# Kernel optimization log

Measured on AMD Instinct MI355X. Metric: run time of the kernel, lower is better.

Reference implementation:

```python
import jax, jax.numpy as jnp
import numpy as np

D = 128          # node_embed_size
N_NODES = 100000
E = 600000       # edges per relation (3 relations)
NEG_SLOPE = 0.01 # F.leaky_relu default


def setup_inputs() -> dict:
    key = jax.random.key(0)
    ks = jax.random.split(key, 17)
    s = 1.0 / np.sqrt(D)
    inp = {
        "N": jax.random.normal(ks[0], (N_NODES, D), jnp.float32),
        # fc1 weights per domain: [D, D] (torch Linear weight layout: out x in)
        "W1_0": jax.random.normal(ks[1], (D, D), jnp.float32) * s,
        "W1_1": jax.random.normal(ks[2], (D, D), jnp.float32) * s,
        "W1_2": jax.random.normal(ks[3], (D, D), jnp.float32) * s,
        # fc2 weights per domain: [1, 2D]
        "w2_0": jax.random.normal(ks[4], (1, 2 * D), jnp.float32) * s,
        "w2_1": jax.random.normal(ks[5], (1, 2 * D), jnp.float32) * s,
        "w2_2": jax.random.normal(ks[6], (1, 2 * D), jnp.float32) * s,
        "Wq": jax.random.normal(ks[7], (D, D), jnp.float32) * s,
        "Wk": jax.random.normal(ks[8], (D, D), jnp.float32) * s,
        "Wv": jax.random.normal(ks[9], (D, D), jnp.float32) * s,
        "src0": jax.random.randint(ks[10], (E,), 0, N_NODES, jnp.int32),
        "dst0": jax.random.randint(ks[11], (E,), 0, N_NODES, jnp.int32),
        "src1": jax.random.randint(ks[12], (E,), 0, N_NODES, jnp.int32),
        "dst1": jax.random.randint(ks[13], (E,), 0, N_NODES, jnp.int32),
        "src2": jax.random.randint(ks[14], (E,), 0, N_NODES, jnp.int32),
        "dst2": jax.random.randint(ks[15], (E,), 0, N_NODES, jnp.int32),
        "target_idx": 0,
    }
    return inp


def _leaky(x):
    return jnp.where(x >= 0, x, NEG_SLOPE * x)


def _gat_relation(N, W1, w2, src, dst, n_nodes):
    # e_edge = leaky_relu(fc2(cat(fc1(N[src]), fc1(N[dst]))))
    # fc2 on a concat == left half dot src part + right half dot dst part,
    # so compute per-node scores once and gather (standard GAT trick).
    d = N.shape[1]
    h = N @ W1.T                      # [n, d]
    sl = h @ w2[0, :d]                # [n]
    sr = h @ w2[0, d:]                # [n]
    e = _leaky(sl[src] + sr[dst])     # [E]
    # segment softmax over edges grouped by destination node (DGL mailbox softmax)
    m = jax.ops.segment_max(e, dst, num_segments=n_nodes)   # [n], -inf for empty
    ex = jnp.exp(e - m[dst])                                 # [E]
    den = jax.ops.segment_sum(ex, dst, num_segments=n_nodes) # [n]
    alpha = ex / den[dst]                                    # [E]
    # weighted sum of source features; zero for nodes with no in-edges
    return jax.ops.segment_sum(alpha[:, None] * N[src], dst, num_segments=n_nodes)


def reference(N, W1_0, W1_1, W1_2, w2_0, w2_1, w2_2, Wq, Wk, Wv,
              src0, dst0, src1, dst1, src2, dst2, target_idx):
    n, d = N.shape
    rels = [(W1_0, w2_0, src0, dst0), (W1_1, w2_1, src1, dst1), (W1_2, w2_2, src2, dst2)]
    h = [_gat_relation(N, W1, w2, src, dst, n) for (W1, w2, src, dst) in rels]
    hs = jnp.stack(h)                         # [3, n, d]
    q = h[target_idx] @ Wq.T                  # [n, d]
    k = jnp.einsum('knd,ed->kne', hs, Wk)     # [3, n, d]
    # (Wv value is computed in the original but never used in the output)
    e = jnp.einsum('nd,knd->nk', q, k) / jnp.sqrt(jnp.asarray(d, N.dtype))  # [n, 3]
    a = jax.nn.softmax(e, axis=1)             # [n, 3]
    Np = jnp.einsum('nk,knd->nd', a, hs)      # [n, d]
    return Np
```

## Files before the change

### kernel.cpp

```cpp
#include <hip/hip_runtime.h>
#include <hip/hip_bf16.h>
#include <math.h>

#define DD 128

typedef __attribute__((ext_vector_type(8))) short short8;
typedef __attribute__((ext_vector_type(4))) float f32x4;

static __device__ __forceinline__ unsigned short f2bf(float f) {
    unsigned u = __float_as_uint(f);
    u += 0x7fffu + ((u >> 16) & 1u);
    return (unsigned short)(u >> 16);
}
static __device__ __forceinline__ float bflo(unsigned mm) { return __uint_as_float(mm << 16); }
static __device__ __forceinline__ float bfhi(unsigned mm) { return __uint_as_float(mm & 0xffff0000u); }

static __device__ __forceinline__ f32x4 MFMA(short8 a, short8 b, f32x4 c) {
    return __builtin_amdgcn_mfma_f32_16x16x32_bf16(a, b, c, 0, 0, 0);
}
static __device__ __forceinline__ int uswz(int u) { return u ^ ((u >> 4) & 7); }

__global__ void k_fill(float* __restrict__ out, float v, int n) {
    int i = blockIdx.x * 256 + threadIdx.x;
    if (i < n) out[i] = v;
}

__global__ void k_prep(const float* __restrict__ Wq, const float* __restrict__ Wk,
                       const float* __restrict__ W10, const float* __restrict__ W11,
                       const float* __restrict__ W12,
                       const float* __restrict__ w20, const float* __restrict__ w21,
                       const float* __restrict__ w22,
                       unsigned short* __restrict__ Bh, unsigned short* __restrict__ Bl,
                       float* __restrict__ uv, unsigned* __restrict__ cnt, int SEG) {
    int b = blockIdx.x, j = threadIdx.x;
    if (b < DD) {
        float acc = 0.f;
        for (int k = 0; k < DD; ++k)
            acc += Wq[k*DD + b] * Wk[k*DD + j];
        unsigned short hi = f2bf(acc);
        unsigned short lo = f2bf(acc - bflo(hi));
        int t  = j >> 4;
        int ks = b >> 5;
        int l  = ((b >> 3) & 3) * 16 + (j & 15);
        int jj = b & 7;
        int idx = ((t*4 + ks)*64 + l)*8 + jj;
        Bh[idx] = hi;
        Bl[idx] = lo;
    } else if (b < DD + 3) {
        int r = b - DD;
        const float* W1 = (r==0) ? W10 : (r==1 ? W11 : W12);
        const float* w2 = (r==0) ? w20 : (r==1 ? w21 : w22);
        float u = 0.f, v = 0.f;
        for (int k = 0; k < DD; ++k) {
            float w = W1[k*DD + j];
            u += w2[k]      * w;
            v += w2[DD + k] * w;
        }
        uv[r*256 + j]      = u;
        uv[r*256 + DD + j] = v;
    } else {
        int idx = (b - (DD + 3)) * DD + j;
        if (idx < SEG) cnt[idx] = 0u;
    }
}

__global__ void __launch_bounds__(256) k_scores(
        const float* __restrict__ N, const float* __restrict__ uv,
        float* __restrict__ sl, float* __restrict__ sr,
        uint2* __restrict__ Nbf, unsigned* __restrict__ cnt,
        unsigned* __restrict__ rank,
        const int* __restrict__ d0, const int* __restrict__ d1,
        const int* __restrict__ d2,
        int n, int E) {
    int tid = threadIdx.x;
    int g = blockIdx.x * 256 + tid;
    if (g < 3*E) {
        int r = (g >= 2*E) ? 2 : (g >= E ? 1 : 0);
        int e = g - r*E;
        const int* Dd = (r==0) ? d0 : (r==1 ? d1 : d2);
        rank[g] = atomicAdd(&cnt[(size_t)r*n + Dd[e]], 1u);
    }
    int wave = tid >> 6, lane = tid & 63, half = lane >> 5, l32 = lane & 31;
    int iw = blockIdx.x * 8 + wave * 2 + half;
    if (iw >= n && blockIdx.x * 8 >= n) return;
    int i = (iw < n) ? iw : (n - 1);
    float4 nv = ((const float4*)N)[(size_t)i * 32 + l32];
    if (iw < n) {
        uint2 pk;
        pk.x = (unsigned)f2bf(nv.x) | ((unsigned)f2bf(nv.y) << 16);
        pk.y = (unsigned)f2bf(nv.z) | ((unsigned)f2bf(nv.w) << 16);
        Nbf[(size_t)iw * 32 + l32] = pk;
    }
    const float4* UV4 = (const float4*)uv;
    float acc[6];
#pragma unroll
    for (int r = 0; r < 3; ++r) {
        float4 u = UV4[r*64 + l32];
        float4 v = UV4[r*64 + 32 + l32];
        acc[2*r]   = nv.x*u.x + nv.y*u.y + nv.z*u.z + nv.w*u.w;
        acc[2*r+1] = nv.x*v.x + nv.y*v.y + nv.z*v.z + nv.w*v.w;
    }
#pragma unroll
    for (int o = 16; o; o >>= 1) {
#pragma unroll
        for (int q = 0; q < 6; ++q) acc[q] += __shfl_xor(acc[q], o);
    }
    if (l32 == 0 && iw < n) {
#pragma unroll
        for (int r = 0; r < 3; ++r) {
            sl[(size_t)r*n + iw] = acc[2*r];
            sr[(size_t)r*n + iw] = acc[2*r+1];
        }
    }
}

__global__ void __launch_bounds__(256) k_scan1(unsigned* __restrict__ off,
                                               unsigned* __restrict__ bsum, int SEG) {
    __shared__ unsigned s[256];
    int tid = threadIdx.x;
    int i = blockIdx.x * 256 + tid;
    unsigned v = (i < SEG) ? off[i] : 0u;
    s[tid] = v; __syncthreads();
#pragma unroll
    for (int o = 1; o < 256; o <<= 1) {
        unsigned a = (tid >= o) ? s[tid - o] : 0u; __syncthreads();
        s[tid] += a; __syncthreads();
    }
    if (i < SEG) off[i] = s[tid] - v;
    if (tid == 255) bsum[blockIdx.x] = s[255];
}

__global__ void __launch_bounds__(256) k_scan2(unsigned* __restrict__ bsum, int nb) {
    __shared__ unsigned s[256];
    __shared__ unsigned carry;
    int tid = threadIdx.x;
    if (tid == 0) carry = 0u;
    for (int base = 0; base < nb; base += 256) {
        int i = base + tid;
        unsigned v = (i < nb) ? bsum[i] : 0u;
        __syncthreads();
        s[tid] = v; __syncthreads();
#pragma unroll
        for (int o = 1; o < 256; o <<= 1) {
            unsigned a = (tid >= o) ? s[tid - o] : 0u; __syncthreads();
            s[tid] += a; __syncthreads();
        }
        unsigned incl = s[tid], tot = s[255], c = carry;
        if (i < nb) bsum[i] = c + incl - v;
        __syncthreads();
        if (tid == 0) carry = c + tot;
    }
}

__global__ void k_scatter(const int* __restrict__ s0, const int* __restrict__ d0,
                          const int* __restrict__ s1, const int* __restrict__ d1,
                          const int* __restrict__ s2, const int* __restrict__ d2,
                          const float* __restrict__ sl, const float* __restrict__ sr,
                          const unsigned* __restrict__ off,
                          const unsigned* __restrict__ bsum,
                          const unsigned* __restrict__ rank,
                          uint2* __restrict__ edat, int n, int E) {
    int g = blockIdx.x * 256 + threadIdx.x;
    if (g >= 3*E) return;
    int r = (g >= 2*E) ? 2 : (g >= E ? 1 : 0);
    int e = g - r*E;
    const int* S  = (r==0) ? s0 : (r==1 ? s1 : s2);
    const int* Dd = (r==0) ? d0 : (r==1 ? d1 : d2);
    int si = S[e], di = Dd[e];
    int seg = r*n + di;
    float x = sl[(size_t)r*n + si] + sr[seg];
    x = (x >= 0.f) ? x : 0.01f * x;
    unsigned p = off[seg] + bsum[seg >> 8] + rank[g];
    edat[p] = make_uint2((unsigned)si, __float_as_uint(x));
}

__global__ void __launch_bounds__(512, 8) k_node(
        const uint4* __restrict__ Nbf,
        const uint4* __restrict__ B4h, const uint4* __restrict__ B4l,
        const unsigned* __restrict__ off,
        const unsigned* __restrict__ bsum,
        const uint2* __restrict__ edat,
        const int* __restrict__ tgt,
        float* __restrict__ out, int n, int TOT) {
    __shared__ uint4 afrag[2][256];
    __shared__ float Tl[16*132];
    int tid = threadIdx.x;
    if (tid < 256 && (tid & 15) >= 8) {
        afrag[0][tid] = make_uint4(0u,0u,0u,0u);
        afrag[1][tid] = make_uint4(0u,0u,0u,0u);
    }
    int wave = tid >> 6, lane = tid & 63, q = lane >> 4, l16 = lane & 15;
    int iw = blockIdx.x * 8 + wave;
    int i = (iw < n) ? iw : (n - 1);
    int t = tgt[0];
    t = (t < 0) ? 0 : (t > 2 ? 2 : t);
    int SEG = 3*n;

    int A[3], C[3];
#pragma unroll
    for (int r = 0; r < 3; ++r) {
        int seg = r*n + i;
        int a = (int)(off[seg] + bsum[seg >> 8]);
        int b = (seg + 1 < SEG) ? (int)(off[seg+1] + bsum[(seg+1) >> 8]) : TOT;
        A[r] = a; C[r] = b - a;
    }

    float m_[3], inv_[3];
#pragma unroll
    for (int r = 0; r < 3; ++r) {
        int cc = C[r];
        float m, s;
        if (cc <= 64) {
            float x = (lane < cc) ? __uint_as_float(edat[A[r] + lane].y) : -INFINITY;
            m = x;
#pragma unroll
            for (int o = 32; o; o >>= 1) m = fmaxf(m, __shfl_xor(m, o));
            s = (lane < cc) ? __expf(x - m) : 0.f;
#pragma unroll
            for (int o = 32; o; o >>= 1) s += __shfl_xor(s, o);
        } else {
            m = -INFINITY;
            for (int j = A[r] + lane; j < A[r] + cc; j += 64)
                m = fmaxf(m, __uint_as_float(edat[j].y));
#pragma unroll
            for (int o = 32; o; o >>= 1) m = fmaxf(m, __shfl_xor(m, o));
            s = 0.f;
            for (int j = A[r] + lane; j < A[r] + cc; j += 64)
                s += __expf(__uint_as_float(edat[j].y) - m);
#pragma unroll
            for (int o = 32; o; o >>= 1) s += __shfl_xor(s, o);
        }
        m_[r] = m; inv_[r] = 1.f / s;
    }

    float hr[3][8];
#pragma unroll
    for (int r = 0; r < 3; ++r) {
        float h[8] = {0.f,0.f,0.f,0.f,0.f,0.f,0.f,0.f};
        int cc = C[r], a = A[r];
        float mm = m_[r], iv = inv_[r];
        for (int p = 0; p < cc; p += 8) {
            int i0 = p + q, i1 = p + 4 + q;
            int e0 = (i0 < cc) ? i0 : cc - 1;
            int e1 = (i1 < cc) ? i1 : cc - 1;
            uint2 d0 = edat[a + e0];
            uint2 d1 = edat[a + e1];
            uint4 v0 = Nbf[(size_t)d0.x * 16 + l16];
            uint4 v1 = Nbf[(size_t)d1.x * 16 + l16];
            float a0 = (i0 < cc) ? __expf(__uint_as_float(d0.y) - mm) * iv : 0.f;
            float a1 = (i1 < cc) ? __expf(__uint_as_float(d1.y) - mm) * iv : 0.f;
            h[0] += a0*bflo(v0.x) + a1*bflo(v1.x);
            h[1] += a0*bfhi(v0.x) + a1*bfhi(v1.x);
            h[2] += a0*bflo(v0.y) + a1*bflo(v1.y);
            h[3] += a0*bfhi(v0.y) + a1*bfhi(v1.y);
            h[4] += a0*bflo(v0.z) + a1*bflo(v1.z);
            h[5] += a0*bfhi(v0.z) + a1*bfhi(v1.z);
            h[6] += a0*bflo(v0.w) + a1*bflo(v1.w);
            h[7] += a0*bfhi(v0.w) + a1*bfhi(v1.w);
        }
#pragma unroll
        for (int k = 0; k < 8; ++k) {
            h[k] += __shfl_xor(h[k], 16);
            h[k] += __shfl_xor(h[k], 32);
            hr[r][k] = h[k];
        }
        if (r == t && lane < 16) {
            unsigned ph[4], pl[4];
#pragma unroll
            for (int k = 0; k < 4; ++k) {
                unsigned short h0 = f2bf(h[2*k]);
                unsigned short h1 = f2bf(h[2*k+1]);
                unsigned short g0 = f2bf(h[2*k]   - bflo(h0));
                unsigned short g1 = f2bf(h[2*k+1] - bflo(h1));
                ph[k] = (unsigned)h0 | ((unsigned)h1 << 16);
                pl[k] = (unsigned)g0 | ((unsigned)g1 << 16);
            }
            int u = uswz(((lane >> 2) * 64) + ((lane & 3) * 16) + wave);
            afrag[0][u] = make_uint4(ph[0], ph[1], ph[2], ph[3]);
            afrag[1][u] = make_uint4(pl[0], pl[1], pl[2], pl[3]);
        }
    }
    __syncthreads();

    {
        f32x4 acc = {0.f, 0.f, 0.f, 0.f};
        for (int ks = 0; ks < 4; ++ks) {
            uint4 a_hi = afrag[0][uswz(ks*64 + lane)];
            uint4 a_lo = afrag[1][uswz(ks*64 + lane)];
            uint4 b_hi = B4h[(wave*4 + ks)*64 + lane];
            uint4 b_lo = B4l[(wave*4 + ks)*64 + lane];
            acc = MFMA(__builtin_bit_cast(short8, a_hi),
                       __builtin_bit_cast(short8, b_hi), acc);
            acc = MFMA(__builtin_bit_cast(short8, a_lo),
                       __builtin_bit_cast(short8, b_hi), acc);
            acc = MFMA(__builtin_bit_cast(short8, a_hi),
                       __builtin_bit_cast(short8, b_lo), acc);
        }
        int col = wave*16 + l16;
#pragma unroll
        for (int rg = 0; rg < 4; ++rg)
            Tl[(q*4 + rg)*132 + col] = acc[rg];
    }
    __syncthreads();

    float4 ta = *(const float4*)&Tl[wave*132 + 8*l16];
    float4 tb = *(const float4*)&Tl[wave*132 + 8*l16 + 4];
    float t8[8] = {ta.x, ta.y, ta.z, ta.w, tb.x, tb.y, tb.z, tb.w};

    const float inv = 0.088388347648318447f;
    float e[3];
#pragma unroll
    for (int r = 0; r < 3; ++r) {
        float v = 0.f;
#pragma unroll
        for (int k = 0; k < 8; ++k) v += t8[k]*hr[r][k];
#pragma unroll
        for (int o = 8; o; o >>= 1) v += __shfl_xor(v, o);
        e[r] = v * inv;
    }
    float mx = fmaxf(e[0], fmaxf(e[1], e[2]));
    float x0 = __expf(e[0]-mx), x1 = __expf(e[1]-mx), x2 = __expf(e[2]-mx);
    float sinv = 1.f / (x0 + x1 + x2);
    float aw0 = x0*sinv, aw1 = x1*sinv, aw2 = x2*sinv;
    if (q == 0 && iw < n) {
        float4 oa, ob;
        oa.x = aw0*hr[0][0] + aw1*hr[1][0] + aw2*hr[2][0];
        oa.y = aw0*hr[0][1] + aw1*hr[1][1] + aw2*hr[2][1];
        oa.z = aw0*hr[0][2] + aw1*hr[1][2] + aw2*hr[2][2];
        oa.w = aw0*hr[0][3] + aw1*hr[1][3] + aw2*hr[2][3];
        ob.x = aw0*hr[0][4] + aw1*hr[1][4] + aw2*hr[2][4];
        ob.y = aw0*hr[0][5] + aw1*hr[1][5] + aw2*hr[2][5];
        ob.z = aw0*hr[0][6] + aw1*hr[1][6] + aw2*hr[2][6];
        ob.w = aw0*hr[0][7] + aw1*hr[1][7] + aw2*hr[2][7];
        ((float4*)(out + (size_t)iw * DD))[2*l16]     = oa;
        ((float4*)(out + (size_t)iw * DD))[2*l16 + 1] = ob;
    }
}

extern "C" void kernel_launch(void* const* d_in, const int* in_sizes, int n_in,
                              void* d_out, int out_size, void* d_ws, size_t ws_size,
                              hipStream_t stream) {
    float* outp = (float*)d_out;
    int fillgrid = (out_size + 255) / 256;
    if (n_in != 17) {
        k_fill<<<fillgrid, 256, 0, stream>>>(outp, 1024.0f, out_size);
        return;
    }
    int n = in_sizes[0] / DD;
    int E = in_sizes[10];
    bool ok = (in_sizes[0] % DD == 0)
        && in_sizes[1]==DD*DD && in_sizes[2]==DD*DD && in_sizes[3]==DD*DD
        && in_sizes[4]==2*DD  && in_sizes[5]==2*DD  && in_sizes[6]==2*DD
        && in_sizes[7]==DD*DD && in_sizes[8]==DD*DD && in_sizes[9]==DD*DD
        && in_sizes[11]==E && in_sizes[12]==E && in_sizes[13]==E
        && in_sizes[14]==E && in_sizes[15]==E && in_sizes[16]==1;
    if (!ok) {
        k_fill<<<fillgrid, 256, 0, stream>>>(outp, 512.0f, out_size);
        return;
    }
    int SEG = 3*n;
    int NB1 = (SEG + 255) / 256;
    int tot = 3*E;

    size_t o_edat = (size_t)2*SEG + 768 + DD*DD + SEG + NB1 + (size_t)tot;
    o_edat = (o_edat + 1) & ~(size_t)1;
    size_t o_nbf = o_edat + (size_t)2*tot;
    o_nbf = (o_nbf + 3) & ~(size_t)3;
    size_t need_f = o_nbf + (size_t)n*64;
    if (ws_size < need_f * sizeof(float)) {
        k_fill<<<fillgrid, 256, 0, stream>>>(outp, 256.0f, out_size);
        return;
    }

    const float* N   = (const float*)d_in[0];
    const float* W10 = (const float*)d_in[1];
    const float* W11 = (const float*)d_in[2];
    const float* W12 = (const float*)d_in[3];
    const float* w20 = (const float*)d_in[4];
    const float* w21 = (const float*)d_in[5];
    const float* w22 = (const float*)d_in[6];
    const float* Wq  = (const float*)d_in[7];
    const float* Wk  = (const float*)d_in[8];
    const int* s0 = (const int*)d_in[10];
    const int* d0 = (const int*)d_in[11];
    const int* s1 = (const int*)d_in[12];
    const int* d1 = (const int*)d_in[13];
    const int* s2 = (const int*)d_in[14];
    const int* d2 = (const int*)d_in[15];
    const int* tgt = (const int*)d_in[16];

    float* ws = (float*)d_ws;
    float* sl = ws;
    float* sr = sl + SEG;
    float* uv = sr + SEG;
    unsigned short* Bh = (unsigned short*)(uv + 768);
    unsigned short* Bl = Bh + DD*DD;
    unsigned* off  = (unsigned*)(uv + 768 + DD*DD);
    unsigned* bsum = off + SEG;
    unsigned* rank = bsum + NB1;
    uint2*    edat = (uint2*)(ws + o_edat);
    unsigned* Nbf  = (unsigned*)(ws + o_nbf);

    int NBZ = (SEG + DD - 1) / DD;
    int gridS = (n + 7) / 8;
    int gridC = (tot + 255) / 256;
    if (gridC > gridS) gridS = gridC;

    k_prep<<<DD + 3 + NBZ, DD, 0, stream>>>(Wq, Wk, W10, W11, W12,
                                            w20, w21, w22, Bh, Bl, uv, off, SEG);
    k_scores<<<gridS, 256, 0, stream>>>(N, uv, sl, sr, (uint2*)Nbf, off, rank,
                                        d0, d1, d2, n, E);
    k_scan1<<<NB1, 256, 0, stream>>>(off, bsum, SEG);
    k_scan2<<<1, 256, 0, stream>>>(bsum, NB1);
    k_scatter<<<(tot + 255)/256, 256, 0, stream>>>(s0,d0,s1,d1,s2,d2, sl,sr,
                                                   off, bsum, rank, edat, n, E);
    k_node<<<(n + 7)/8, 512, 0, stream>>>((const uint4*)Nbf,
                                          (const uint4*)Bh, (const uint4*)Bl,
                                          off, bsum, edat, tgt, outp, n, tot);
}
```

Measured before the change: 426.9 us.

## Process two nodes per wavefront in node kernel using half-wave lanes

Each 64-lane wave now handles two destination nodes, one per 32-lane half, so a 512-thread block covers 16 nodes and the MFMA tile is fully populated. The softmax reductions and the gather loop are remapped to 32 lanes with two edges per step per half. With about six in-edges per node per relation, the intent is to cut idle lanes and halve the block count. In exchange, each half processes fewer edges in parallel per step, and the zero-padding of unused afrag rows is dropped because all 16 rows are now filled.

```diff
diff --git a/kernel.cpp b/kernel.cpp
--- a/kernel.cpp
+++ b/kernel.cpp
@@ -185,12 +185,13 @@
     __shared__ uint4 afrag[2][256];
     __shared__ float Tl[16*132];
     int tid = threadIdx.x;
-    if (tid < 256 && (tid & 15) >= 8) {
-        afrag[0][tid] = make_uint4(0u,0u,0u,0u);
-        afrag[1][tid] = make_uint4(0u,0u,0u,0u);
-    }
-    int wave = tid >> 6, lane = tid & 63, q = lane >> 4, l16 = lane & 15;
-    int iw = blockIdx.x * 8 + wave;
+    int wave = tid >> 6, lane = tid & 63;
+    int half = lane >> 5;
+    int l32 = lane & 31;
+    int g2 = (lane >> 4) & 1;
+    int l16 = lane & 15;
+    int nid = wave * 2 + half;
+    int iw = blockIdx.x * 16 + nid;
     int i = (iw < n) ? iw : (n - 1);
     int t = tgt[0];
     t = (t < 0) ? 0 : (t > 2 ? 2 : t);
@@ -210,25 +211,25 @@
     for (int r = 0; r < 3; ++r) {
         int cc = C[r];
         float m, s;
-        if (cc <= 64) {
-            float x = (lane < cc) ? __uint_as_float(edat[A[r] + lane].y) : -INFINITY;
+        if (cc <= 32) {
+            float x = (l32 < cc) ? __uint_as_float(edat[A[r] + l32].y) : -INFINITY;
             m = x;
 #pragma unroll
-            for (int o = 32; o; o >>= 1) m = fmaxf(m, __shfl_xor(m, o));
-            s = (lane < cc) ? __expf(x - m) : 0.f;
-#pragma unroll
-            for (int o = 32; o; o >>= 1) s += __shfl_xor(s, o);
+            for (int o = 16; o; o >>= 1) m = fmaxf(m, __shfl_xor(m, o));
+            s = (l32 < cc) ? __expf(x - m) : 0.f;
+#pragma unroll
+            for (int o = 16; o; o >>= 1) s += __shfl_xor(s, o);
         } else {
             m = -INFINITY;
-            for (int j = A[r] + lane; j < A[r] + cc; j += 64)
+            for (int j = A[r] + l32; j < A[r] + cc; j += 32)
                 m = fmaxf(m, __uint_as_float(edat[j].y));
 #pragma unroll
-            for (int o = 32; o; o >>= 1) m = fmaxf(m, __shfl_xor(m, o));
+            for (int o = 16; o; o >>= 1) m = fmaxf(m, __shfl_xor(m, o));
             s = 0.f;
-            for (int j = A[r] + lane; j < A[r] + cc; j += 64)
+            for (int j = A[r] + l32; j < A[r] + cc; j += 32)
                 s += __expf(__uint_as_float(edat[j].y) - m);
 #pragma unroll
-            for (int o = 32; o; o >>= 1) s += __shfl_xor(s, o);
+            for (int o = 16; o; o >>= 1) s += __shfl_xor(s, o);
         }
         m_[r] = m; inv_[r] = 1.f / s;
     }
@@ -239,8 +240,8 @@
         float h[8] = {0.f,0.f,0.f,0.f,0.f,0.f,0.f,0.f};
         int cc = C[r], a = A[r];
         float mm = m_[r], iv = inv_[r];
-        for (int p = 0; p < cc; p += 8) {
-            int i0 = p + q, i1 = p + 4 + q;
+        for (int p = 0; p < cc; p += 4) {
+            int i0 = p + g2, i1 = p + 2 + g2;
             int e0 = (i0 < cc) ? i0 : cc - 1;
             int e1 = (i1 < cc) ? i1 : cc - 1;
             uint2 d0 = edat[a + e0];
@@ -261,10 +262,9 @@
 #pragma unroll
         for (int k = 0; k < 8; ++k) {
             h[k] += __shfl_xor(h[k], 16);
-            h[k] += __shfl_xor(h[k], 32);
             hr[r][k] = h[k];
         }
-        if (r == t && lane < 16) {
+        if (r == t && l32 < 16) {
             unsigned ph[4], pl[4];
 #pragma unroll
             for (int k = 0; k < 4; ++k) {
@@ -275,7 +275,7 @@
                 ph[k] = (unsigned)h0 | ((unsigned)h1 << 16);
                 pl[k] = (unsigned)g0 | ((unsigned)g1 << 16);
             }
-            int u = uswz(((lane >> 2) * 64) + ((lane & 3) * 16) + wave);
+            int u = uswz(((l16 >> 2) * 64) + ((l16 & 3) * 16) + nid);
             afrag[0][u] = make_uint4(ph[0], ph[1], ph[2], ph[3]);
             afrag[1][u] = make_uint4(pl[0], pl[1], pl[2], pl[3]);
         }
@@ -283,6 +283,7 @@
     __syncthreads();
 
     {
+        int qm = lane >> 4;
         f32x4 acc = {0.f, 0.f, 0.f, 0.f};
         for (int ks = 0; ks < 4; ++ks) {
             uint4 a_hi = afrag[0][uswz(ks*64 + lane)];
@@ -299,12 +300,12 @@
         int col = wave*16 + l16;
 #pragma unroll
         for (int rg = 0; rg < 4; ++rg)
-            Tl[(q*4 + rg)*132 + col] = acc[rg];
+            Tl[(qm*4 + rg)*132 + col] = acc[rg];
     }
     __syncthreads();
 
-    float4 ta = *(const float4*)&Tl[wave*132 + 8*l16];
-    float4 tb = *(const float4*)&Tl[wave*132 + 8*l16 + 4];
+    float4 ta = *(const float4*)&Tl[nid*132 + 8*l16];
+    float4 tb = *(const float4*)&Tl[nid*132 + 8*l16 + 4];
     float t8[8] = {ta.x, ta.y, ta.z, ta.w, tb.x, tb.y, tb.z, tb.w};
 
     const float inv = 0.088388347648318447f;
@@ -322,7 +323,7 @@
     float x0 = __expf(e[0]-mx), x1 = __expf(e[1]-mx), x2 = __expf(e[2]-mx);
     float sinv = 1.f / (x0 + x1 + x2);
     float aw0 = x0*sinv, aw1 = x1*sinv, aw2 = x2*sinv;
-    if (q == 0 && iw < n) {
+    if (g2 == 0 && iw < n) {
         float4 oa, ob;
         oa.x = aw0*hr[0][0] + aw1*hr[1][0] + aw2*hr[2][0];
         oa.y = aw0*hr[0][1] + aw1*hr[1][1] + aw2*hr[2][1];
@@ -414,7 +415,7 @@
     k_scan2<<<1, 256, 0, stream>>>(bsum, NB1);
     k_scatter<<<(tot + 255)/256, 256, 0, stream>>>(s0,d0,s1,d1,s2,d2, sl,sr,
                                                    off, bsum, rank, edat, n, E);
-    k_node<<<(n + 7)/8, 512, 0, stream>>>((const uint4*)Nbf,
-                                          (const uint4*)Bh, (const uint4*)Bl,
-                                          off, bsum, edat, tgt, outp, n, tot);
-}
+    k_node<<<(n + 15)/16, 512, 0, stream>>>((const uint4*)Nbf,
+                                            (const uint4*)Bh, (const uint4*)Bl,
+                                            off, bsum, edat, tgt, outp, n, tot);
+}
```

Result: faster. 394.9 us (-7.5%).
